# Optimization experiments

Measured on AMD Instinct MI355X. Metric: run time of the kernel, lower is better.

## Reference

```python
import jax, jax.numpy as jnp
import numpy as np

OUT_FEATURES = 4096
IN_FEATURES = 4096

# NF4 codebook (bitsandbytes normal-float 4-bit values)
_NF4_CODEBOOK = np.array([
    -1.0, -0.6961928, -0.52507305, -0.3949175, -0.28444138, -0.18477343,
    -0.09105004, 0.0, 0.0795803, 0.1609302, 0.2461123, 0.33791524,
    0.44070983, 0.562617, 0.72295684, 1.0], dtype=np.float32)


def setup_inputs() -> dict:
    key = jax.random.key(0)
    k_x, k_codes, k_scale, k_bias = jax.random.split(key, 4)
    x = jax.random.normal(k_x, (4, 2048, IN_FEATURES), dtype=jnp.float32)
    # packed uint8 nibble codes stored as int32 in [0, 256)
    packed_codes = jax.random.randint(
        k_codes, (OUT_FEATURES * IN_FEATURES // 2,), 0, 256, dtype=jnp.int32)
    # positive per-channel scales [out, 1]
    scale = jax.random.uniform(k_scale, (OUT_FEATURES, 1), dtype=jnp.float32) * 0.05 + 0.01
    bias = jax.random.normal(k_bias, (OUT_FEATURES,), dtype=jnp.float32)
    return {"x": x, "packed_codes": packed_codes, "scale": scale, "bias": bias}


def _dequantize_nf4(packed_codes, scale):
    codebook = jnp.asarray(_NF4_CODEBOOK)
    low = packed_codes & 15           # even positions
    high = (packed_codes >> 4) & 15   # odd positions
    # interleave: unpacked[0::2]=low, unpacked[1::2]=high
    idx = jnp.stack([low, high], axis=-1).reshape(-1)  # [out*in]
    w = codebook[idx].reshape(OUT_FEATURES, IN_FEATURES) * scale  # [out, in]
    return w


def reference(x, packed_codes, scale, bias):
    w = _dequantize_nf4(packed_codes, scale)
    # F.linear: x @ w.T + bias
    return jnp.einsum("bsi,oi->bso", x, w) + bias
```

## Files before the change

### kernel.cpp

```cpp
#include <hip/hip_runtime.h>
#include <stdint.h>

#define IN_F 4096
#define OUT_F 4096
#define M_ROWS 8192

__device__ __constant__ int c_nf4_i8[16] = {
    -127, -88, -67, -50, -36, -23, -12, 0, 10, 20, 31, 43, 56, 71, 92, 127};

typedef int i32x4 __attribute__((ext_vector_type(4)));
typedef int i32x16 __attribute__((ext_vector_type(16)));

__global__ __launch_bounds__(256) void k_quant_x(
    const float* __restrict__ x, signed char* __restrict__ xq,
    float* __restrict__ steps) {
  const int row = blockIdx.x;
  const int tid = threadIdx.x;
  const float4* xr = (const float4*)(x + (size_t)row * IN_F);
  float4 v[4];
  float m = 0.0f;
#pragma unroll
  for (int i = 0; i < 4; ++i) {
    v[i] = xr[tid + 256 * i];
    m = fmaxf(m, fmaxf(fmaxf(fabsf(v[i].x), fabsf(v[i].y)),
                       fmaxf(fabsf(v[i].z), fabsf(v[i].w))));
  }
#pragma unroll
  for (int off = 32; off > 0; off >>= 1) m = fmaxf(m, __shfl_xor(m, off));
  __shared__ float wmax[4];
  if ((tid & 63) == 0) wmax[tid >> 6] = m;
  __syncthreads();
  m = fmaxf(fmaxf(wmax[0], wmax[1]), fmaxf(wmax[2], wmax[3]));
  const float inv = (m > 0.0f) ? 127.0f / m : 0.0f;
  if (tid == 0) steps[row] = m * (1.0f / 127.0f);
  int* oq = (int*)(xq + (size_t)row * IN_F);
#pragma unroll
  for (int i = 0; i < 4; ++i) {
    int q0 = (int)rintf(v[i].x * inv);
    int q1 = (int)rintf(v[i].y * inv);
    int q2 = (int)rintf(v[i].z * inv);
    int q3 = (int)rintf(v[i].w * inv);
    oq[tid + 256 * i] =
        (q0 & 255) | ((q1 & 255) << 8) | ((q2 & 255) << 16) | (q3 << 24);
  }
}

__global__ __launch_bounds__(256) void k_dequant(
    const int* __restrict__ packed, signed char* __restrict__ W) {
  __shared__ short lut[256];
  {
    const int b = threadIdx.x;
    const int lo = c_nf4_i8[b & 15], hi = c_nf4_i8[b >> 4];
    lut[b] = (short)((lo & 0xFF) | ((hi & 0xFF) << 8));
  }
  __syncthreads();
  const int tid = blockIdx.x * 256 + threadIdx.x;
  const int4 ca = ((const int4*)packed)[2 * tid];
  const int4 cb = ((const int4*)packed)[2 * tid + 1];
  union { short h[8]; int4 v; } o;
  o.h[0] = lut[ca.x]; o.h[1] = lut[ca.y]; o.h[2] = lut[ca.z]; o.h[3] = lut[ca.w];
  o.h[4] = lut[cb.x]; o.h[5] = lut[cb.y]; o.h[6] = lut[cb.z]; o.h[7] = lut[cb.w];
  ((int4*)W)[tid] = o.v;
}

#define GLL(gptr, lptr)                                          \
  __builtin_amdgcn_global_load_lds(                              \
      (__attribute__((address_space(1))) void*)(gptr),           \
      (__attribute__((address_space(3))) void*)(lptr), 16, 0, 0)

#define FENCE() asm volatile("" ::: "memory")

__device__ __forceinline__ void gemm_phase(
    const signed char* SA, const signed char* SB, const int ks,
    const int wm, const int wn, const int r31, const int khalf,
    const int ln7, const int w, i32x16 (&acc)[4][2],
    const signed char* gsrc, signed char* ldst, const int kt,
    const int doStage, const int waitZero) {
  i32x4 af[4], bf[2];
  const int ch = ((2 * ks + khalf) ^ ln7) * 16;
#pragma unroll
  for (int f = 0; f < 4; ++f)
    af[f] = *(const i32x4*)&SA[(wm * 128 + f * 32 + r31) * 128 + ch];
#pragma unroll
  for (int g = 0; g < 2; ++g)
    bf[g] = *(const i32x4*)&SB[(wn * 64 + g * 32 + r31) * 128 + ch];
  if (doStage) {
#pragma unroll
    for (int st = 0; st < 4; ++st)
      GLL(gsrc + (size_t)(st * 64) * IN_F + (size_t)kt * 128,
          ldst + (st * 64 + w * 8) * 128);
  }
  FENCE();
  __builtin_amdgcn_s_barrier();
  FENCE();
  __builtin_amdgcn_s_setprio(1);
#pragma unroll
  for (int f = 0; f < 4; ++f)
#pragma unroll
    for (int g = 0; g < 2; ++g)
      acc[f][g] =
          __builtin_amdgcn_mfma_i32_32x32x32_i8(af[f], bf[g], acc[f][g], 0, 0, 0);
  __builtin_amdgcn_s_setprio(0);
  if (waitZero) asm volatile("s_waitcnt vmcnt(0)" ::: "memory");
  FENCE();
  __builtin_amdgcn_s_barrier();
  FENCE();
}

__global__ __launch_bounds__(512, 2) void k_gemm(
    const signed char* __restrict__ A,
    const signed char* __restrict__ B,
    const float* __restrict__ steps,
    const float* __restrict__ scale,
    const float* __restrict__ bias,
    float* __restrict__ C) {
  __shared__ __align__(16) signed char sA[2][256 * 128];
  __shared__ __align__(16) signed char sB[2][256 * 128];
  const int tid = threadIdx.x;
  const int lane = tid & 63;
  const int w = tid >> 6;
  const int wm = w >> 2;
  const int wn = w & 3;
  const int r31 = lane & 31;
  const int khalf = lane >> 5;
  const int ln7 = lane & 7;

  const int orig = blockIdx.x;
  const int swz = (orig & 7) * 64 + (orig >> 3);
  const int bn = (swz & 15) * 256;
  const int bm = (swz >> 4) * 256;

  const int tr = w * 8 + (lane >> 3);
  const int schnk = (lane & 7) ^ (lane >> 3);
  const signed char* gA = A + (size_t)(bm + tr) * IN_F + schnk * 16;
  const signed char* gB = B + (size_t)(bn + tr) * IN_F + schnk * 16;

  i32x16 acc[4][2] = {};

  auto stage4 = [&](const signed char* gsrc, signed char* ldst, int kt) {
#pragma unroll
    for (int st = 0; st < 4; ++st)
      GLL(gsrc + (size_t)(st * 64) * IN_F + (size_t)kt * 128,
          ldst + (st * 64 + w * 8) * 128);
  };

  stage4(gA, &sA[0][0], 0);
  stage4(gB, &sB[0][0], 0);
  stage4(gA, &sA[1][0], 1);
  stage4(gB, &sB[1][0], 1);
  asm volatile("s_waitcnt vmcnt(8)" ::: "memory");
  FENCE();
  __builtin_amdgcn_s_barrier();
  FENCE();

#pragma unroll 1
  for (int it = 0; it < 16; ++it) {
    const int stY = (it > 0);
    const int stX = (it < 15);
    const int kY = 2 * it + 1;
    const int kX = 2 * it + 2;
    gemm_phase(sA[0], sB[0], 0, wm, wn, r31, khalf, ln7, w, acc,
               gA, &sA[1][0], kY, stY, 0);
    gemm_phase(sA[0], sB[0], 1, wm, wn, r31, khalf, ln7, w, acc,
               gB, &sB[1][0], kY, stY, 0);
    gemm_phase(sA[0], sB[0], 2, wm, wn, r31, khalf, ln7, w, acc,
               gA, &sA[0][0], 0, 0, 0);
    gemm_phase(sA[0], sB[0], 3, wm, wn, r31, khalf, ln7, w, acc,
               gA, &sA[0][0], 0, 0, 1);
    gemm_phase(sA[1], sB[1], 0, wm, wn, r31, khalf, ln7, w, acc,
               gA, &sA[0][0], kX, stX, 0);
    gemm_phase(sA[1], sB[1], 1, wm, wn, r31, khalf, ln7, w, acc,
               gB, &sB[0][0], kX, stX, 0);
    gemm_phase(sA[1], sB[1], 2, wm, wn, r31, khalf, ln7, w, acc,
               gA, &sA[0][0], 0, 0, 0);
    gemm_phase(sA[1], sB[1], 3, wm, wn, r31, khalf, ln7, w, acc,
               gA, &sA[0][0], 0, 0, 1);
  }

#pragma unroll
  for (int f = 0; f < 4; ++f) {
    const int row0 = bm + wm * 128 + f * 32 + 4 * khalf;
#pragma unroll
    for (int g = 0; g < 2; ++g) {
      const int col = bn + wn * 64 + g * 32 + r31;
      const float fc = scale[col] * (1.0f / 127.0f);
      const float bv = bias[col];
#pragma unroll
      for (int reg = 0; reg < 16; ++reg) {
        const int row = row0 + (reg & 3) + 8 * (reg >> 2);
        C[(size_t)row * OUT_F + col] =
            (float)acc[f][g][reg] * (steps[row] * fc) + bv;
      }
    }
  }
}

extern "C" void kernel_launch(void* const* d_in, const int* in_sizes, int n_in,
                              void* d_out, int out_size, void* d_ws, size_t ws_size,
                              hipStream_t stream) {
  const float* x      = (const float*)d_in[0];
  const int* packed   = (const int*)d_in[1];
  const float* scale  = (const float*)d_in[2];
  const float* bias   = (const float*)d_in[3];
  float* out = (float*)d_out;

  signed char* Xq = (signed char*)d_ws;
  signed char* Wq = Xq + (size_t)M_ROWS * IN_F;
  float* steps = (float*)(Wq + (size_t)OUT_F * IN_F);

  k_quant_x<<<M_ROWS, 256, 0, stream>>>(x, Xq, steps);
  k_dequant<<<(OUT_F * IN_F / 2) / (256 * 8), 256, 0, stream>>>(packed, Wq);
  k_gemm<<<(OUT_F / 256) * (M_ROWS / 256), 512, 0, stream>>>(
      Xq, Wq, steps, scale, bias, out);
}
```

Baseline: 378.7 us.

## Restructure GEMM main loop to one barrier per K-tile with register double-buffering

Replaces the eight-phase main loop, which had two workgroup barriers per K-substep, with a per-tile routine. Each tile issues the async global-to-LDS copies for the next tile once, then alternates LDS fragment loads and MFMA groups using two register fragment sets. It ends with a single wait and barrier. The prologue now preloads only the first tile and waits for it fully. The aim is to cut barrier and synchronization overhead so more LDS reads overlap with MFMAs, at the cost of higher register pressure and a shallower prefetch lead.

New measurement: 378.5 us. No clear change (-0.1%).

```diff
diff --git a/kernel.cpp b/kernel.cpp
--- a/kernel.cpp
+++ b/kernel.cpp
@@ -69,43 +69,6 @@
       (__attribute__((address_space(3))) void*)(lptr), 16, 0, 0)
 
 #define FENCE() asm volatile("" ::: "memory")
-
-__device__ __forceinline__ void gemm_phase(
-    const signed char* SA, const signed char* SB, const int ks,
-    const int wm, const int wn, const int r31, const int khalf,
-    const int ln7, const int w, i32x16 (&acc)[4][2],
-    const signed char* gsrc, signed char* ldst, const int kt,
-    const int doStage, const int waitZero) {
-  i32x4 af[4], bf[2];
-  const int ch = ((2 * ks + khalf) ^ ln7) * 16;
-#pragma unroll
-  for (int f = 0; f < 4; ++f)
-    af[f] = *(const i32x4*)&SA[(wm * 128 + f * 32 + r31) * 128 + ch];
-#pragma unroll
-  for (int g = 0; g < 2; ++g)
-    bf[g] = *(const i32x4*)&SB[(wn * 64 + g * 32 + r31) * 128 + ch];
-  if (doStage) {
-#pragma unroll
-    for (int st = 0; st < 4; ++st)
-      GLL(gsrc + (size_t)(st * 64) * IN_F + (size_t)kt * 128,
-          ldst + (st * 64 + w * 8) * 128);
-  }
-  FENCE();
-  __builtin_amdgcn_s_barrier();
-  FENCE();
-  __builtin_amdgcn_s_setprio(1);
-#pragma unroll
-  for (int f = 0; f < 4; ++f)
-#pragma unroll
-    for (int g = 0; g < 2; ++g)
-      acc[f][g] =
-          __builtin_amdgcn_mfma_i32_32x32x32_i8(af[f], bf[g], acc[f][g], 0, 0, 0);
-  __builtin_amdgcn_s_setprio(0);
-  if (waitZero) asm volatile("s_waitcnt vmcnt(0)" ::: "memory");
-  FENCE();
-  __builtin_amdgcn_s_barrier();
-  FENCE();
-}
 
 __global__ __launch_bounds__(512, 2) void k_gemm(
     const signed char* __restrict__ A,
@@ -144,37 +107,60 @@
           ldst + (st * 64 + w * 8) * 128);
   };
 
+  auto ldfrag = [&](i32x4 (&af)[4], i32x4 (&bf)[2], const signed char* SA_,
+                    const signed char* SB_, int ks) {
+    const int ch = ((2 * ks + khalf) ^ ln7) * 16;
+#pragma unroll
+    for (int f = 0; f < 4; ++f)
+      af[f] = *(const i32x4*)&SA_[(wm * 128 + f * 32 + r31) * 128 + ch];
+#pragma unroll
+    for (int g = 0; g < 2; ++g)
+      bf[g] = *(const i32x4*)&SB_[(wn * 64 + g * 32 + r31) * 128 + ch];
+  };
+
+  auto mfma8 = [&](i32x4 (&af)[4], i32x4 (&bf)[2]) {
+    __builtin_amdgcn_s_setprio(1);
+#pragma unroll
+    for (int f = 0; f < 4; ++f)
+#pragma unroll
+      for (int g = 0; g < 2; ++g)
+        acc[f][g] = __builtin_amdgcn_mfma_i32_32x32x32_i8(af[f], bf[g],
+                                                          acc[f][g], 0, 0, 0);
+    __builtin_amdgcn_s_setprio(0);
+  };
+
+  auto tile = [&](const signed char* SA_, const signed char* SB_,
+                  signed char* dA, signed char* dB, int tnext, int doStage) {
+    i32x4 aX[4], bX[2], aY[4], bY[2];
+    ldfrag(aX, bX, SA_, SB_, 0);
+    ldfrag(aY, bY, SA_, SB_, 1);
+    if (doStage) {
+      stage4(gA, dA, tnext);
+      stage4(gB, dB, tnext);
+    }
+    mfma8(aX, bX);
+    ldfrag(aX, bX, SA_, SB_, 2);
+    mfma8(aY, bY);
+    ldfrag(aY, bY, SA_, SB_, 3);
+    mfma8(aX, bX);
+    mfma8(aY, bY);
+    if (doStage) asm volatile("s_waitcnt vmcnt(0)" ::: "memory");
+    FENCE();
+    __builtin_amdgcn_s_barrier();
+    FENCE();
+  };
+
   stage4(gA, &sA[0][0], 0);
   stage4(gB, &sB[0][0], 0);
-  stage4(gA, &sA[1][0], 1);
-  stage4(gB, &sB[1][0], 1);
-  asm volatile("s_waitcnt vmcnt(8)" ::: "memory");
+  asm volatile("s_waitcnt vmcnt(0)" ::: "memory");
   FENCE();
   __builtin_amdgcn_s_barrier();
   FENCE();
 
 #pragma unroll 1
-  for (int it = 0; it < 16; ++it) {
-    const int stY = (it > 0);
-    const int stX = (it < 15);
-    const int kY = 2 * it + 1;
-    const int kX = 2 * it + 2;
-    gemm_phase(sA[0], sB[0], 0, wm, wn, r31, khalf, ln7, w, acc,
-               gA, &sA[1][0], kY, stY, 0);
-    gemm_phase(sA[0], sB[0], 1, wm, wn, r31, khalf, ln7, w, acc,
-               gB, &sB[1][0], kY, stY, 0);
-    gemm_phase(sA[0], sB[0], 2, wm, wn, r31, khalf, ln7, w, acc,
-               gA, &sA[0][0], 0, 0, 0);
-    gemm_phase(sA[0], sB[0], 3, wm, wn, r31, khalf, ln7, w, acc,
-               gA, &sA[0][0], 0, 0, 1);
-    gemm_phase(sA[1], sB[1], 0, wm, wn, r31, khalf, ln7, w, acc,
-               gA, &sA[0][0], kX, stX, 0);
-    gemm_phase(sA[1], sB[1], 1, wm, wn, r31, khalf, ln7, w, acc,
-               gB, &sB[0][0], kX, stX, 0);
-    gemm_phase(sA[1], sB[1], 2, wm, wn, r31, khalf, ln7, w, acc,
-               gA, &sA[0][0], 0, 0, 0);
-    gemm_phase(sA[1], sB[1], 3, wm, wn, r31, khalf, ln7, w, acc,
-               gA, &sA[0][0], 0, 0, 1);
+  for (int t2 = 0; t2 < 32; t2 += 2) {
+    tile(&sA[0][0], &sB[0][0], &sA[1][0], &sB[1][0], t2 + 1, 1);
+    tile(&sA[1][0], &sB[1][0], &sA[0][0], &sB[0][0], t2 + 2, (t2 + 2 < 32));
   }
 
 #pragma unroll
```
